# Kernel optimization log

Measured on AMD Instinct MI355X. Metric: run time of the kernel, lower is better.

The kernel has to match this reference:

```python
import jax, jax.numpy as jnp
import numpy as np
import math

B, S, H, K = 512, 200, 256, 16

def setup_inputs() -> dict:
    key = jax.random.key(0)
    ks = jax.random.split(key, 8)
    scale = 1.0 / math.sqrt(H)
    return {
        "input_tensor": jax.random.normal(ks[0], (B, S, H), dtype=jnp.float32),
        "item_mask": jax.random.randint(ks[1], (B, S, 1), 0, 2) > 0,
        "time_f_w_matrix": jax.random.uniform(ks[2], (B, S, 1), dtype=jnp.float32),
        "W1": jax.random.normal(ks[3], (H, H), dtype=jnp.float32) * scale,
        "b1": jnp.zeros((H,), dtype=jnp.float32),
        "W2": jax.random.normal(ks[4], (H, H), dtype=jnp.float32) * scale,
        "b2": jnp.zeros((H,), dtype=jnp.float32),
        "W3": jax.random.normal(ks[5], (H, K), dtype=jnp.float32) * scale,
    }

def reference(input_tensor, item_mask, time_f_w_matrix, W1, b1, W2, b2, W3):
    # small MLP: two Linear+ReLU then bias-free Linear to k_interests
    h = jax.nn.relu(jnp.einsum('bsh,hd->bsd', input_tensor, W1) + b1)
    h = jax.nn.relu(jnp.einsum('bsh,hd->bsd', h, W2) + b2)
    D = jnp.einsum('bsh,hk->bsk', h, W3)              # [B,S,K]
    D = jax.nn.softmax(D, axis=-1)                    # softmax over interests
    mask = item_mask[:, :, 0:1]                       # [B,S,1] bool, broadcast over K
    D = jnp.where(mask, D, jnp.float32(-10000.0))
    D = D / jnp.float32(math.sqrt(K))
    D = jax.nn.softmax(D, axis=-2)                    # softmax over sequence
    D = time_f_w_matrix[:, :, 0:1] * D                # time weighting
    # einsum 'nij,nik->nkj': pool items into K interest vectors
    return jnp.einsum('bsh,bsk->bkh', input_tensor, D)
```

## Files before the change

### kernel.cpp

```cpp
#include <hip/hip_runtime.h>
#include <math.h>

#define HDIM 256
#define KDIM 16
#define SDIM 200
#define BDIM 512
#define NROWS (BDIM * SDIM)
#define TM 32

typedef __bf16 bf16x8 __attribute__((ext_vector_type(8)));
typedef __bf16 bf16x4 __attribute__((ext_vector_type(4)));
typedef float  f32x4  __attribute__((ext_vector_type(4)));

__global__ __launch_bounds__(256) void pack_all(
    const float* __restrict__ W1, const float* __restrict__ W2,
    const float* __restrict__ W3,
    __bf16* __restrict__ w1h, __bf16* __restrict__ w1l,
    __bf16* __restrict__ w2h, __bf16* __restrict__ w2l,
    __bf16* __restrict__ w3h, __bf16* __restrict__ w3l)
{
    int gid = blockIdx.x * 256 + threadIdx.x;
    const float* src;
    __bf16 *oh, *ol;
    int e, N;
    if (gid < 65536)       { src = W1; oh = w1h; ol = w1l; e = gid;          N = 256; }
    else if (gid < 131072) { src = W2; oh = w2h; ol = w2l; e = gid - 65536;  N = 256; }
    else if (gid < 135168) { src = W3; oh = w3h; ol = w3l; e = gid - 131072; N = 16;  }
    else return;

    int j  = e & 7;
    int n  = (e >> 3) & (N - 1);
    int kg = e >> 3; kg = (N == 256) ? (kg >> 8) : (kg >> 4);
    int k  = kg * 8 + j;
    float v = src[k * N + n];
    __bf16 h = (__bf16)v;
    oh[e] = h;
    ol[e] = (__bf16)(v - (float)h);
}

__global__ __launch_bounds__(256) void mlp_softk_mfma(
    const float* __restrict__ X, const int* __restrict__ mask,
    const __bf16* __restrict__ W1h, const __bf16* __restrict__ W1l,
    const float* __restrict__ b1,
    const __bf16* __restrict__ W2h, const __bf16* __restrict__ W2l,
    const float* __restrict__ b2,
    const __bf16* __restrict__ W3h, const __bf16* __restrict__ W3l,
    float* __restrict__ P)
{
    __shared__ __bf16 Ahi[TM * HDIM];
    __shared__ __bf16 Alo[TM * HDIM];

    const int tid  = threadIdx.x;
    const int lane = tid & 63;
    const int w    = tid >> 6;
    const int l15  = lane & 15;
    const int quad = lane >> 4;
    const long r0  = (long)blockIdx.x * TM;

    {
        const float4* Xt = (const float4*)(X + r0 * HDIM);
        #pragma unroll
        for (int t = 0; t < (TM * HDIM / 4) / 256; ++t) {
            int v4  = tid + t * 256;
            float4 f = Xt[v4];
            int row = v4 >> 6;
            int col = (v4 & 63) << 2;
            int kgs = (col >> 3) ^ (row & 31);
            int base = row * HDIM + kgs * 8 + (col & 7);
            __bf16 h0 = (__bf16)f.x, h1 = (__bf16)f.y,
                   h2 = (__bf16)f.z, h3 = (__bf16)f.w;
            bf16x4 hv = {h0, h1, h2, h3};
            bf16x4 lv = {(__bf16)(f.x - (float)h0), (__bf16)(f.y - (float)h1),
                         (__bf16)(f.z - (float)h2), (__bf16)(f.w - (float)h3)};
            *(bf16x4*)(&Ahi[base]) = hv;
            *(bf16x4*)(&Alo[base]) = lv;
        }
    }
    __syncthreads();

    f32x4 acc[2][4];

    auto layer = [&](const __bf16* __restrict__ Wh, const __bf16* __restrict__ Wl,
                     const float* __restrict__ bias) {
        #pragma unroll
        for (int mt = 0; mt < 2; ++mt)
            #pragma unroll
            for (int nt = 0; nt < 4; ++nt)
                acc[mt][nt] = (f32x4){0.f, 0.f, 0.f, 0.f};

        #pragma unroll
        for (int kc = 0; kc < 8; ++kc) {
            bf16x8 bh[4], bl[4], ah[2], al[2];
            #pragma unroll
            for (int nt = 0; nt < 4; ++nt) {
                int n  = w * 64 + nt * 16 + l15;
                int kg = kc * 4 + quad;
                bh[nt] = *(const bf16x8*)(Wh + (kg * HDIM + n) * 8);
                bl[nt] = *(const bf16x8*)(Wl + (kg * HDIM + n) * 8);
            }
            #pragma unroll
            for (int mt = 0; mt < 2; ++mt) {
                int row = mt * 16 + l15;
                int kgs = (kc * 4 + quad) ^ (row & 31);
                ah[mt] = *(const bf16x8*)(&Ahi[row * HDIM + kgs * 8]);
                al[mt] = *(const bf16x8*)(&Alo[row * HDIM + kgs * 8]);
            }
            #pragma unroll
            for (int mt = 0; mt < 2; ++mt)
                #pragma unroll
                for (int nt = 0; nt < 4; ++nt) {
                    acc[mt][nt] = __builtin_amdgcn_mfma_f32_16x16x32_bf16(
                        bh[nt], ah[mt], acc[mt][nt], 0, 0, 0);
                    acc[mt][nt] = __builtin_amdgcn_mfma_f32_16x16x32_bf16(
                        bh[nt], al[mt], acc[mt][nt], 0, 0, 0);
                    acc[mt][nt] = __builtin_amdgcn_mfma_f32_16x16x32_bf16(
                        bl[nt], ah[mt], acc[mt][nt], 0, 0, 0);
                }
        }
        __syncthreads();

        f32x4 bias4[4];
        #pragma unroll
        for (int nt = 0; nt < 4; ++nt)
            bias4[nt] = *(const f32x4*)(bias + w * 64 + nt * 16 + quad * 4);

        #pragma unroll
        for (int mt = 0; mt < 2; ++mt)
            #pragma unroll
            for (int nt = 0; nt < 4; ++nt) {
                int m   = mt * 16 + l15;
                int g   = w * 8 + nt * 2 + (quad >> 1);
                int idx = m * HDIM + ((g ^ (m & 31)) * 8) + (quad & 1) * 4;
                bf16x4 hv, lv;
                #pragma unroll
                for (int r = 0; r < 4; ++r) {
                    float v = fmaxf(acc[mt][nt][r] + bias4[nt][r], 0.f);
                    __bf16 h = (__bf16)v;
                    hv[r] = h;
                    lv[r] = (__bf16)(v - (float)h);
                }
                *(bf16x4*)(&Ahi[idx]) = hv;
                *(bf16x4*)(&Alo[idx]) = lv;
            }
        __syncthreads();
    };

    layer(W1h, W1l, b1);
    layer(W2h, W2l, b2);

    if (w < 2) {
        f32x4 lg = {0.f, 0.f, 0.f, 0.f};
        #pragma unroll
        for (int kc = 0; kc < 8; ++kc) {
            int row = w * 16 + l15;
            int kg  = kc * 4 + quad;
            int kgs = kg ^ (row & 31);
            bf16x8 ah = *(const bf16x8*)(&Ahi[row * HDIM + kgs * 8]);
            bf16x8 al = *(const bf16x8*)(&Alo[row * HDIM + kgs * 8]);
            bf16x8 bh = *(const bf16x8*)(W3h + (kg * KDIM + l15) * 8);
            bf16x8 bl = *(const bf16x8*)(W3l + (kg * KDIM + l15) * 8);
            lg = __builtin_amdgcn_mfma_f32_16x16x32_bf16(ah, bh, lg, 0, 0, 0);
            lg = __builtin_amdgcn_mfma_f32_16x16x32_bf16(al, bh, lg, 0, 0, 0);
            lg = __builtin_amdgcn_mfma_f32_16x16x32_bf16(ah, bl, lg, 0, 0, 0);
        }

        #pragma unroll
        for (int r = 0; r < 4; ++r) {
            float v  = lg[r];
            float mx = v;
            mx = fmaxf(mx, __shfl_xor(mx, 1));
            mx = fmaxf(mx, __shfl_xor(mx, 2));
            mx = fmaxf(mx, __shfl_xor(mx, 4));
            mx = fmaxf(mx, __shfl_xor(mx, 8));
            float e = __expf(v - mx);
            float s = e;
            s += __shfl_xor(s, 1);
            s += __shfl_xor(s, 2);
            s += __shfl_xor(s, 4);
            s += __shfl_xor(s, 8);
            int grow = (int)r0 + w * 16 + quad * 4 + r;
            int mv   = mask[grow];
            float ov = mv ? (e / s) * 0.25f : -2500.0f;
            P[(long)grow * KDIM + l15] = ov;
        }
    }
}

__global__ __launch_bounds__(512) void softs_agg_kernel(
    const float* __restrict__ X, const float* __restrict__ tf,
    const float* __restrict__ P, float* __restrict__ out)
{
    __shared__ float wl[SDIM * KDIM];
    __shared__ float tfl[SDIM];
    __shared__ float invk[KDIM];
    __shared__ float red[6 * 8 * HDIM];
    float* psum = red;

    const int tid = threadIdx.x;
    const int b   = blockIdx.x;

    const float* Pb = P + (long)b * SDIM * KDIM;
    float ps = 0.f;
    #pragma unroll
    for (int t = 0; t < 7; ++t) {
        int i = tid + t * 512;
        if (i < SDIM * KDIM) {
            float e = __expf(Pb[i]);
            wl[i] = e;
            ps += e;
        }
    }
    psum[tid] = ps;
    if (tid < SDIM) tfl[tid] = tf[b * SDIM + tid];
    __syncthreads();

    if (tid < KDIM) {
        float s = 0.f;
        #pragma unroll
        for (int g = 0; g < 32; ++g) s += psum[tid + g * 16];
        invk[tid] = 1.f / s;
    }
    __syncthreads();

    #pragma unroll
    for (int t = 0; t < 7; ++t) {
        int i = tid + t * 512;
        if (i < SDIM * KDIM) wl[i] *= tfl[i >> 4] * invk[i & 15];
    }
    __syncthreads();

    const int wv = tid >> 6;
    const int sq = wv >> 1;
    const int kh = wv & 1;
    const int ln = tid & 63;

    f32x4 acc[8];
    #pragma unroll
    for (int j = 0; j < 8; ++j) acc[j] = (f32x4){0.f, 0.f, 0.f, 0.f};

    const f32x4* Xb4 = (const f32x4*)(X + (long)b * SDIM * HDIM);
    const f32x4* wl4 = (const f32x4*)wl;
    const int s0 = sq * 50;
    #pragma unroll 5
    for (int si = 0; si < 50; ++si) {
        int s = s0 + si;
        f32x4 x  = Xb4[s * 64 + ln];
        f32x4 d0 = wl4[s * 4 + 2 * kh + 0];
        f32x4 d1 = wl4[s * 4 + 2 * kh + 1];
        #pragma unroll
        for (int j = 0; j < 4; ++j) {
            acc[j]     += x * d0[j];
            acc[4 + j] += x * d1[j];
        }
    }

    if (sq > 0) {
        float* rp = red + (((sq - 1) * 2 + kh) * 8) * HDIM;
        #pragma unroll
        for (int j = 0; j < 8; ++j)
            *(f32x4*)(rp + j * HDIM + 4 * ln) = acc[j];
    }
    __syncthreads();
    if (sq == 0) {
        #pragma unroll
        for (int p = 0; p < 3; ++p) {
            const float* rp = red + ((p * 2 + kh) * 8) * HDIM;
            #pragma unroll
            for (int j = 0; j < 8; ++j)
                acc[j] += *(const f32x4*)(rp + j * HDIM + 4 * ln);
        }
        float* ob = out + (long)b * KDIM * HDIM + kh * 8 * HDIM;
        #pragma unroll
        for (int j = 0; j < 8; ++j)
            *(f32x4*)(ob + j * HDIM + 4 * ln) = acc[j];
    }
}

extern "C" void kernel_launch(void* const* d_in, const int* in_sizes, int n_in,
                              void* d_out, int out_size, void* d_ws, size_t ws_size,
                              hipStream_t stream) {
    (void)in_sizes; (void)n_in; (void)out_size; (void)ws_size;
    const float* X    = (const float*)d_in[0];
    const int*   mask = (const int*)  d_in[1];
    const float* tf   = (const float*)d_in[2];
    const float* W1   = (const float*)d_in[3];
    const float* b1   = (const float*)d_in[4];
    const float* W2   = (const float*)d_in[5];
    const float* b2   = (const float*)d_in[6];
    const float* W3   = (const float*)d_in[7];
    float* out = (float*)d_out;

    char* ws = (char*)d_ws;
    float*  P   = (float*)ws;
    __bf16* w1h = (__bf16*)(ws + 6553600);
    __bf16* w1l = w1h + 65536;
    __bf16* w2h = w1l + 65536;
    __bf16* w2l = w2h + 65536;
    __bf16* w3h = w2l + 65536;
    __bf16* w3l = w3h + 4096;

    pack_all<<<528, 256, 0, stream>>>(W1, W2, W3, w1h, w1l, w2h, w2l, w3h, w3l);
    mlp_softk_mfma<<<NROWS / TM, 256, 0, stream>>>(X, mask, w1h, w1l, b1,
                                                   w2h, w2l, b2, w3h, w3l, P);
    softs_agg_kernel<<<BDIM, 512, 0, stream>>>(X, tf, P, out);
}
```

Before: 263.0 us.

## Interleave hi/lo weight packs and double-buffer weight fragment loads in MLP layers

The weight packing now stores the bf16 hi and lo halves of W1/W2 next to each other (16 bf16 per k-group and column), so each lane fetches both with one contiguous 32-byte access. The MLP layer loop also prefetches the next k-chunk's weight fragments into a second register buffer while MFMAs run on the current one, to hide global/L2 load latency. This uses more VGPRs for the doubled fragment arrays, which could lower occupancy.

```diff
diff --git a/kernel.cpp b/kernel.cpp
--- a/kernel.cpp
+++ b/kernel.cpp
@@ -15,35 +15,38 @@
 __global__ __launch_bounds__(256) void pack_all(
     const float* __restrict__ W1, const float* __restrict__ W2,
     const float* __restrict__ W3,
-    __bf16* __restrict__ w1h, __bf16* __restrict__ w1l,
-    __bf16* __restrict__ w2h, __bf16* __restrict__ w2l,
+    __bf16* __restrict__ w1i, __bf16* __restrict__ w2i,
     __bf16* __restrict__ w3h, __bf16* __restrict__ w3l)
 {
     int gid = blockIdx.x * 256 + threadIdx.x;
-    const float* src;
-    __bf16 *oh, *ol;
-    int e, N;
-    if (gid < 65536)       { src = W1; oh = w1h; ol = w1l; e = gid;          N = 256; }
-    else if (gid < 131072) { src = W2; oh = w2h; ol = w2l; e = gid - 65536;  N = 256; }
-    else if (gid < 135168) { src = W3; oh = w3h; ol = w3l; e = gid - 131072; N = 16;  }
-    else return;
-
-    int j  = e & 7;
-    int n  = (e >> 3) & (N - 1);
-    int kg = e >> 3; kg = (N == 256) ? (kg >> 8) : (kg >> 4);
-    int k  = kg * 8 + j;
-    float v = src[k * N + n];
-    __bf16 h = (__bf16)v;
-    oh[e] = h;
-    ol[e] = (__bf16)(v - (float)h);
+    if (gid < 131072) {
+        int sel = gid >> 16;
+        int e   = gid & 65535;
+        const float* src = sel ? W2 : W1;
+        __bf16*      dst = sel ? w2i : w1i;
+        int j  = e & 7;
+        int n  = (e >> 3) & 255;
+        int kg = e >> 11;
+        float v  = src[(kg * 8 + j) * 256 + n];
+        __bf16 h = (__bf16)v;
+        dst[(kg * 256 + n) * 16 + j]     = h;
+        dst[(kg * 256 + n) * 16 + 8 + j] = (__bf16)(v - (float)h);
+    } else if (gid < 135168) {
+        int e  = gid - 131072;
+        int j  = e & 7;
+        int n  = (e >> 3) & 15;
+        int kg = e >> 7;
+        float v  = W3[(kg * 8 + j) * 16 + n];
+        __bf16 h = (__bf16)v;
+        w3h[e] = h;
+        w3l[e] = (__bf16)(v - (float)h);
+    }
 }
 
 __global__ __launch_bounds__(256) void mlp_softk_mfma(
     const float* __restrict__ X, const int* __restrict__ mask,
-    const __bf16* __restrict__ W1h, const __bf16* __restrict__ W1l,
-    const float* __restrict__ b1,
-    const __bf16* __restrict__ W2h, const __bf16* __restrict__ W2l,
-    const float* __restrict__ b2,
+    const __bf16* __restrict__ W1i, const float* __restrict__ b1,
+    const __bf16* __restrict__ W2i, const float* __restrict__ b2,
     const __bf16* __restrict__ W3h, const __bf16* __restrict__ W3l,
     float* __restrict__ P)
 {
@@ -80,42 +83,51 @@
 
     f32x4 acc[2][4];
 
-    auto layer = [&](const __bf16* __restrict__ Wh, const __bf16* __restrict__ Wl,
-                     const float* __restrict__ bias) {
+    auto layer = [&](const __bf16* __restrict__ Wi, const float* __restrict__ bias) {
         #pragma unroll
         for (int mt = 0; mt < 2; ++mt)
             #pragma unroll
             for (int nt = 0; nt < 4; ++nt)
                 acc[mt][nt] = (f32x4){0.f, 0.f, 0.f, 0.f};
 
+        bf16x8 fh[2][4], fl[2][4];
+        #pragma unroll
+        for (int nt = 0; nt < 4; ++nt) {
+            int n = w * 64 + nt * 16 + l15;
+            const __bf16* p = Wi + ((long)(quad * HDIM + n)) * 16;
+            fh[0][nt] = *(const bf16x8*)(p);
+            fl[0][nt] = *(const bf16x8*)(p + 8);
+        }
+
         #pragma unroll
         for (int kc = 0; kc < 8; ++kc) {
-            bf16x8 bh[4], bl[4], ah[2], al[2];
-            #pragma unroll
-            for (int nt = 0; nt < 4; ++nt) {
-                int n  = w * 64 + nt * 16 + l15;
-                int kg = kc * 4 + quad;
-                bh[nt] = *(const bf16x8*)(Wh + (kg * HDIM + n) * 8);
-                bl[nt] = *(const bf16x8*)(Wl + (kg * HDIM + n) * 8);
+            const int cur = kc & 1;
+            const int nxt = cur ^ 1;
+            if (kc < 7) {
+                #pragma unroll
+                for (int nt = 0; nt < 4; ++nt) {
+                    int n = w * 64 + nt * 16 + l15;
+                    const __bf16* p = Wi + ((long)(((kc + 1) * 4 + quad) * HDIM + n)) * 16;
+                    fh[nxt][nt] = *(const bf16x8*)(p);
+                    fl[nxt][nt] = *(const bf16x8*)(p + 8);
+                }
             }
             #pragma unroll
             for (int mt = 0; mt < 2; ++mt) {
                 int row = mt * 16 + l15;
                 int kgs = (kc * 4 + quad) ^ (row & 31);
-                ah[mt] = *(const bf16x8*)(&Ahi[row * HDIM + kgs * 8]);
-                al[mt] = *(const bf16x8*)(&Alo[row * HDIM + kgs * 8]);
-            }
-            #pragma unroll
-            for (int mt = 0; mt < 2; ++mt)
+                bf16x8 ah = *(const bf16x8*)(&Ahi[row * HDIM + kgs * 8]);
+                bf16x8 al = *(const bf16x8*)(&Alo[row * HDIM + kgs * 8]);
                 #pragma unroll
                 for (int nt = 0; nt < 4; ++nt) {
                     acc[mt][nt] = __builtin_amdgcn_mfma_f32_16x16x32_bf16(
-                        bh[nt], ah[mt], acc[mt][nt], 0, 0, 0);
+                        fh[cur][nt], ah, acc[mt][nt], 0, 0, 0);
                     acc[mt][nt] = __builtin_amdgcn_mfma_f32_16x16x32_bf16(
-                        bh[nt], al[mt], acc[mt][nt], 0, 0, 0);
+                        fh[cur][nt], al, acc[mt][nt], 0, 0, 0);
                     acc[mt][nt] = __builtin_amdgcn_mfma_f32_16x16x32_bf16(
-                        bl[nt], ah[mt], acc[mt][nt], 0, 0, 0);
+                        fl[cur][nt], ah, acc[mt][nt], 0, 0, 0);
                 }
+            }
         }
         __syncthreads();
 
@@ -130,7 +142,7 @@
             for (int nt = 0; nt < 4; ++nt) {
                 int m   = mt * 16 + l15;
                 int g   = w * 8 + nt * 2 + (quad >> 1);
-                int idx = m * HDIM + ((g ^ (m & 31)) * 8) + (quad & 1) * 4;
+                int idx = m * HDIM + (((g ^ (m & 31)) * 8) + (quad & 1) * 4);
                 bf16x4 hv, lv;
                 #pragma unroll
                 for (int r = 0; r < 4; ++r) {
@@ -145,8 +157,8 @@
         __syncthreads();
     };
 
-    layer(W1h, W1l, b1);
-    layer(W2h, W2l, b2);
+    layer(W1i, b1);
+    layer(W2i, b2);
 
     if (w < 2) {
         f32x4 lg = {0.f, 0.f, 0.f, 0.f};
@@ -292,15 +304,13 @@
 
     char* ws = (char*)d_ws;
     float*  P   = (float*)ws;
-    __bf16* w1h = (__bf16*)(ws + 6553600);
-    __bf16* w1l = w1h + 65536;
-    __bf16* w2h = w1l + 65536;
-    __bf16* w2l = w2h + 65536;
-    __bf16* w3h = w2l + 65536;
+    __bf16* w1i = (__bf16*)(ws + 6553600);
+    __bf16* w2i = w1i + 131072;
+    __bf16* w3h = w2i + 131072;
     __bf16* w3l = w3h + 4096;
 
-    pack_all<<<528, 256, 0, stream>>>(W1, W2, W3, w1h, w1l, w2h, w2l, w3h, w3l);
-    mlp_softk_mfma<<<NROWS / TM, 256, 0, stream>>>(X, mask, w1h, w1l, b1,
-                                                   w2h, w2l, b2, w3h, w3l, P);
+    pack_all<<<528, 256, 0, stream>>>(W1, W2, W3, w1i, w2i, w3h, w3l);
+    mlp_softk_mfma<<<NROWS / TM, 256, 0, stream>>>(X, mask, w1i, b1,
+                                                   w2i, b2, w3h, w3l, P);
     softs_agg_kernel<<<BDIM, 512, 0, stream>>>(X, tf, P, out);
 }
```

Result: no change. 263.8 us (+0.3%).
